# Optimization experiments

Hardware: AMD Instinct MI355X
Metric: run time of the kernel (lower is better)

The kernel has to match this reference:

```python
import jax, jax.numpy as jnp
import numpy as np

B, S, D = 4, 4096, 64   # batch, seq_len, input_size
H, HD = 4, 16           # num_heads, head_dim


def setup_inputs() -> dict:
    key = jax.random.key(0)
    ks = jax.random.split(key, 9)
    sd = 1.0 / np.sqrt(D)          # torch Linear default uniform(-1/sqrt(fan_in), ...)
    so = 1.0 / np.sqrt(H * HD)
    u = lambda k, shape, s: jax.random.uniform(k, shape, jnp.float32, -s, s)
    return {
        "x": jax.random.normal(ks[0], (B, S, D), jnp.float32),
        "Wq": u(ks[1], (H, D, HD), sd), "bq": u(ks[2], (H, HD), sd),
        "Wk": u(ks[3], (H, D, HD), sd), "bk": u(ks[4], (H, HD), sd),
        "Wv": u(ks[5], (H, D, HD), sd), "bv": u(ks[6], (H, HD), sd),
        "Wo": u(ks[7], (H * HD, D), so), "bo": u(ks[8], (D,), so),
    }


def reference(x, Wq, bq, Wk, bk, Wv, bv, Wo, bo):
    # Batched per-head projections (fuses the original per-head Linear loop)
    q = jnp.einsum('bsd,hde->bhse', x, Wq) + bq[None, :, None, :]
    k = jnp.einsum('bsd,hde->bhse', x, Wk) + bk[None, :, None, :]
    v = jnp.einsum('bsd,hde->bhse', x, Wv) + bv[None, :, None, :]
    # scores: [B, H, S(query), S(key)]
    scores = jnp.einsum('bhse,bhte->bhst', q, k) / np.sqrt(HD).astype(np.float32)
    # FAITHFUL quirk: torch Softmax(dim=1) on [B,S,S] normalizes over the QUERY axis
    w = jax.nn.softmax(scores, axis=2)
    attended = jnp.einsum('bhst,bhte->bhse', w, v)          # [B,H,S,HD]
    concat = attended.transpose(0, 2, 1, 3).reshape(B, S, H * HD)
    out = concat @ Wo + bo                                   # [B,S,D]
    # FAITHFUL quirk: final softmax over the sequence axis (dim=1)
    return jax.nn.softmax(out, axis=1)
```

## Files before the change

### kernel.cpp

```cpp
#include <hip/hip_runtime.h>
#include <hip/hip_bf16.h>


#define BB 4
#define SS 4096
#define DD 64
#define HH 4
#define HDD 16

typedef unsigned int u32;
typedef unsigned short u16;
typedef __attribute__((ext_vector_type(8))) short bfrag;
typedef __attribute__((ext_vector_type(4))) float floatx4;
typedef __attribute__((ext_vector_type(16))) float floatx16;
typedef __attribute__((ext_vector_type(2))) u32 u32x2;
typedef __attribute__((ext_vector_type(4))) u32 u32x4;

#define LOG2E 1.4426950408889634074f
#define QSCALE (LOG2E * 0.25f)

__device__ __forceinline__ float fexp2(float x) {
#if __has_builtin(__builtin_amdgcn_exp2f)
  return __builtin_amdgcn_exp2f(x);
#else
  float r; asm("v_exp_f32 %0, %1" : "=v"(r) : "v"(x)); return r;
#endif
}
__device__ __forceinline__ float frcp(float x) {
#if __has_builtin(__builtin_amdgcn_rcpf)
  return __builtin_amdgcn_rcpf(x);
#else
  float r; asm("v_rcp_f32 %0, %1" : "=v"(r) : "v"(x)); return r;
#endif
}

__device__ __forceinline__ u16 f2bf(float f) {
  u32 u = __builtin_bit_cast(u32, f);
  return (u16)((u + 0x7FFFu + ((u >> 16) & 1u)) >> 16);
}
__device__ __forceinline__ u32 pack_bf(float lo, float hi) {
#if __has_builtin(__builtin_amdgcn_perm)
  return __builtin_amdgcn_perm(__builtin_bit_cast(u32, hi),
                               __builtin_bit_cast(u32, lo), 0x07060302u);
#else
  u32 a = __builtin_bit_cast(u32, lo);
  u32 b = __builtin_bit_cast(u32, hi);
  return (a >> 16) | (b & 0xFFFF0000u);
#endif
}

__device__ __forceinline__ void gload_lds16(const u16* g, u16* l) {
  __builtin_amdgcn_global_load_lds(
      (const __attribute__((address_space(1))) void*)(g),
      (__attribute__((address_space(3))) void*)(l), 16, 0, 0);
}

__device__ __forceinline__ int tmap(int c) {
  int c5 = c & 31;
  return (c & ~31) + (c5 & 3) + ((c5 >> 2) & 1) * 8 + ((c5 >> 3) & 1) * 16
       + ((c5 >> 4) & 1) * 4;
}

__global__ __launch_bounds__(256) void k_proj(
    const float* __restrict__ x,
    const float* __restrict__ Wq, const float* __restrict__ bq,
    const float* __restrict__ Wk, const float* __restrict__ bk,
    const float* __restrict__ Wv, const float* __restrict__ bv,
    u16* __restrict__ qb, u16* __restrict__ kb, float* __restrict__ vf)
{
  __shared__ float xs[16 * 64];
  const int tid = threadIdx.x;
  const int blk = blockIdx.x;
  const int b   = blk >> 8;
  const int s0  = (blk & 255) << 4;
  ((float4*)xs)[tid] = ((const float4*)(x + ((size_t)b * SS + s0) * DD))[tid];
  __syncthreads();

  const int col = tid & 63, h = col >> 4, e = col & 15;
  const int rg  = tid >> 6;
  float aq[4] = {0,0,0,0}, ak[4] = {0,0,0,0}, av[4] = {0,0,0,0};
  const int wofs = h * (DD * HDD) + e;
#pragma unroll 4
  for (int d = 0; d < DD; ++d) {
    float wq = Wq[wofs + d * HDD];
    float wk = Wk[wofs + d * HDD];
    float wv = Wv[wofs + d * HDD];
    const float* xr = xs + (rg * 4) * 64 + d;
#pragma unroll
    for (int r = 0; r < 4; ++r) {
      float xv = xr[r * 64];
      aq[r] += xv * wq; ak[r] += xv * wk; av[r] += xv * wv;
    }
  }
  const float bqv = bq[col], bkv = bk[col], bvv = bv[col];
  size_t base = ((size_t)(b * HH + h) * SS + (s0 + rg * 4)) * HDD + e;
#pragma unroll
  for (int r = 0; r < 4; ++r) {
    qb[base + r * HDD] = f2bf((aq[r] + bqv) * QSCALE);
    kb[base + r * HDD] = f2bf(ak[r] + bkv);
    vf[base + r * HDD] = av[r] + bvv;
  }
}

__global__ __launch_bounds__(256, 8) void k_colsum(
    const u16* __restrict__ qb, const u16* __restrict__ kb,
    float* __restrict__ csp)
{
  const int tid = threadIdx.x;
  const int lane = tid & 63, w = tid >> 6;
  const int l31 = lane & 31, hl = lane >> 5;
  const int bh = blockIdx.z, chunk = blockIdx.y;
  const int t0 = blockIdx.x * 128 + w * 32;
  const size_t base = (size_t)bh * (SS * HDD);

  const bfrag kf = *(const bfrag*)(kb + base + (size_t)(t0 + l31) * HDD + hl * 8);
  const u16* qp = qb + base + (size_t)l31 * HDD + hl * 8;
  const floatx16 z16 = {0.f};
  float c0 = 0.f, c1 = 0.f, c2 = 0.f, c3 = 0.f;
  const int s0 = chunk * 1024;
#pragma unroll 2
  for (int s = s0; s < s0 + 1024; s += 32) {
    bfrag qfr = *(const bfrag*)(qp + (size_t)s * HDD);
    floatx16 d = __builtin_amdgcn_mfma_f32_32x32x16_bf16(qfr, kf, z16, 0, 0, 0);
#pragma unroll
    for (int i = 0; i < 4; ++i) {
      c0 += fexp2(d[4 * i + 0]);
      c1 += fexp2(d[4 * i + 1]);
      c2 += fexp2(d[4 * i + 2]);
      c3 += fexp2(d[4 * i + 3]);
    }
  }
  float c = (c0 + c1) + (c2 + c3);
  c += __shfl_xor(c, 32, 64);
  if (hl == 0)
    csp[((size_t)bh * 4 + chunk) * SS + t0 + l31] = c;
}

__global__ __launch_bounds__(256) void k_vprep(
    const float* __restrict__ vf, const float* __restrict__ csp,
    u16* __restrict__ vp)
{
  __shared__ float rcls[256];
  const int tid = threadIdx.x;
  const int chunk = blockIdx.x;
  const int bh = blockIdx.y;
  const int t0 = chunk << 8;
  {
    const float* cp = csp + (size_t)bh * 4 * SS + t0 + tid;
    rcls[tid] = frcp(cp[0] + cp[SS] + cp[2 * SS] + cp[3 * SS]);
  }
  __syncthreads();
  const float* vb = vf + ((size_t)bh * SS + t0) * HDD;
  u16* outb = vp + ((size_t)bh * 16 + chunk) * 4096;
#pragma unroll
  for (int gi = 0; gi < 2; ++gi) {
    const int g = gi * 256 + tid;
    const int e = g >> 5, gg = g & 31;
    const int cbase = (gg ^ (e & 7)) << 3;
    u32 r[4];
#pragma unroll
    for (int jj = 0; jj < 4; ++jj) {
      int ta = tmap(cbase + 2 * jj);
      int tb = tmap(cbase + 2 * jj + 1);
      u16 lo = f2bf(vb[ta * HDD + e] * rcls[ta]);
      u16 hi = f2bf(vb[tb * HDD + e] * rcls[tb]);
      r[jj] = (u32)lo | ((u32)hi << 16);
    }
    u32x4 vv = {r[0], r[1], r[2], r[3]};
    *(u32x4*)(outb + g * 8) = vv;
  }
}

__global__ __launch_bounds__(256, 8) void k_attn(
    const u16* __restrict__ qb, const u16* __restrict__ kb,
    const u16* __restrict__ vp, float* __restrict__ attp)
{
  __shared__ __align__(16) u16 vls[2][4096];
  const int tid  = threadIdx.x;
  const int lane = tid & 63, w = tid >> 6;
  const int l31 = lane & 31, hl = lane >> 5;
  const int bh = blockIdx.z, b = bh >> 2, h = bh & 3;
  const int tq = blockIdx.y;
  const int s0 = blockIdx.x * 128 + w * 32;
  const size_t base = (size_t)bh * (SS * HDD);

  const bfrag qf = *(const bfrag*)(qb + base + (size_t)(s0 + l31) * HDD + hl * 8);
  const u16* kp = kb + base + ((size_t)tq * 1024 + l31) * HDD + hl * 8;
  const floatx16 z16 = {0.f};
  floatx16 acc = {0.f};

  const u16* vsrc = vp + ((size_t)bh * 16 + tq * 4) * 4096;

  {
    const u16* gs = vsrc + w * 1024 + lane * 8;
    u16* ls = &vls[0][0] + w * 1024;
    gload_lds16(gs, ls);
    gload_lds16(gs + 512, ls + 512);
  }
  __syncthreads();

#pragma unroll
  for (int ch = 0; ch < 4; ++ch) {
    if (ch < 3) {
      const u16* gs = vsrc + (ch + 1) * 4096 + w * 1024 + lane * 8;
      u16* ls = &vls[(ch + 1) & 1][0] + w * 1024;
      gload_lds16(gs, ls);
      gload_lds16(gs + 512, ls + 512);
    }

    const u16* vrow = &vls[ch & 1][0] + (l31 & 15) * 256;
    const int eb = l31 & 7;
    const int tb = ch * 256;
#pragma unroll 2
    for (int it = 0; it < 8; ++it) {
      bfrag kf = *(const bfrag*)(kp + (size_t)(tb + it * 32) * HDD);
      floatx16 d = __builtin_amdgcn_mfma_f32_32x32x16_bf16(kf, qf, z16, 0, 0, 0);
      u32 wr[8];
#pragma unroll
      for (int p = 0; p < 8; ++p)
        wr[p] = pack_bf(fexp2(d[2 * p]), fexp2(d[2 * p + 1]));
      const int cc0 = it * 4 + hl * 2;
      u32x4 af0 = *(const u32x4*)(vrow + ((cc0 ^ eb) << 3));
      u32x4 af1 = *(const u32x4*)(vrow + (((cc0 + 1) ^ eb) << 3));
      u32x4 ef0 = {wr[0], wr[1], wr[2], wr[3]};
      u32x4 ef1 = {wr[4], wr[5], wr[6], wr[7]};
      acc = __builtin_amdgcn_mfma_f32_32x32x16_bf16(
          __builtin_bit_cast(bfrag, af0), __builtin_bit_cast(bfrag, ef0), acc, 0, 0, 0);
      acc = __builtin_amdgcn_mfma_f32_32x32x16_bf16(
          __builtin_bit_cast(bfrag, af1), __builtin_bit_cast(bfrag, ef1), acc, 0, 0, 0);
    }
    __syncthreads();
  }

  float* ao = attp + (((size_t)tq * BB + b) * SS + s0 + l31) * (HH * HDD)
            + h * HDD + 4 * hl;
  float4 lo4 = {acc[0], acc[1], acc[2], acc[3]};
  float4 hi4 = {acc[4], acc[5], acc[6], acc[7]};
  *(float4*)ao       = lo4;
  *(float4*)(ao + 8) = hi4;
}

__global__ __launch_bounds__(256) void k_oproj(
    const float* __restrict__ att, const float* __restrict__ Wo,
    const float* __restrict__ bo, float* __restrict__ outp,
    float* __restrict__ part)
{
  __shared__ float wols[64 * 64];
  __shared__ float red[4][64];
  const int tid = threadIdx.x;
  const int blk = blockIdx.x;
  const int b = blk >> 9, s0 = (blk & 511) << 3;
#pragma unroll
  for (int i = 0; i < 4; ++i)
    ((float4*)wols)[tid + 256 * i] = ((const float4*)Wo)[tid + 256 * i];
  __syncthreads();

  const int d = tid & 63, sg = tid >> 6;
  const float bov = bo[d];
  const size_t so = (size_t)BB * SS * 16;
  float es = 0.f;
#pragma unroll
  for (int r = 0; r < 2; ++r) {
    int s = s0 + sg * 2 + r;
    const floatx4* row = (const floatx4*)(att + ((size_t)b * SS + s) * 64);
    float acc = bov;
#pragma unroll
    for (int j = 0; j < 16; ++j) {
      floatx4 c = (row[j] + row[j + so]) + (row[j + 2 * so] + row[j + 3 * so]);
      acc += c[0] * wols[(4*j+0)*64 + d] + c[1] * wols[(4*j+1)*64 + d]
           + c[2] * wols[(4*j+2)*64 + d] + c[3] * wols[(4*j+3)*64 + d];
    }
    outp[((size_t)b * SS + s) * 64 + d] = acc;
    es += fexp2(acc * LOG2E);
  }
  red[sg][d] = es;
  __syncthreads();
  if (tid < 64)
    part[((size_t)b * 512 + (blk & 511)) * 64 + tid] =
        red[0][tid] + red[1][tid] + red[2][tid] + red[3][tid];
}

__global__ __launch_bounds__(256) void k_softmax(
    const float* __restrict__ outp, const float* __restrict__ part,
    float* __restrict__ out)
{
  __shared__ float red[4][64];
  __shared__ float rs[64];
  const int tid = threadIdx.x, d = tid & 63, sg = tid >> 6;
  const int st = blockIdx.x;
  const int b = blockIdx.y;
  {
    float e = 0.f;
    const float* pp = part + ((size_t)b * 512 + sg * 128) * 64 + d;
#pragma unroll 8
    for (int c = 0; c < 128; ++c) e += pp[c * 64];
    red[sg][d] = e;
  }
  __syncthreads();
  if (tid < 64)
    rs[tid] = frcp(red[0][tid] + red[1][tid] + red[2][tid] + red[3][tid]);
  __syncthreads();
  const float r = rs[d];
  const size_t rowbase = ((size_t)b * SS + st * 64 + sg * 16) * 64 + d;
#pragma unroll 4
  for (int i = 0; i < 16; ++i)
    out[rowbase + i * 64] = fexp2(outp[rowbase + i * 64] * LOG2E) * r;
}

extern "C" void kernel_launch(void* const* d_in, const int* in_sizes, int n_in,
                              void* d_out, int out_size, void* d_ws, size_t ws_size,
                              hipStream_t stream) {
  const float* x  = (const float*)d_in[0];
  const float* Wq = (const float*)d_in[1];
  const float* bq = (const float*)d_in[2];
  const float* Wk = (const float*)d_in[3];
  const float* bk = (const float*)d_in[4];
  const float* Wv = (const float*)d_in[5];
  const float* bv = (const float*)d_in[6];
  const float* Wo = (const float*)d_in[7];
  const float* bo = (const float*)d_in[8];

  char* ws = (char*)d_ws;
  constexpr size_t QB_OFF  = 0;
  constexpr size_t KB_OFF  = (size_t)2  << 20;
  constexpr size_t VF_OFF  = (size_t)4  << 20;
  constexpr size_t CSP_OFF = (size_t)8  << 20;
  constexpr size_t VP_OFF  = (size_t)9  << 20;
  constexpr size_t ATT_OFF = (size_t)11 << 20;
  constexpr size_t OUT_OFF = (size_t)27 << 20;
  constexpr size_t PT_OFF  = (size_t)31 << 20;

  u16*   qb   = (u16*)  (ws + QB_OFF);
  u16*   kb   = (u16*)  (ws + KB_OFF);
  float* vf   = (float*)(ws + VF_OFF);
  float* csp  = (float*)(ws + CSP_OFF);
  u16*   vpb  = (u16*)  (ws + VP_OFF);
  float* attp = (float*)(ws + ATT_OFF);
  float* outp = (float*)(ws + OUT_OFF);
  float* part = (float*)(ws + PT_OFF);
  float* out  = (float*)d_out;

  hipLaunchKernelGGL(k_proj,    dim3(1024),       dim3(256), 0, stream,
                     x, Wq, bq, Wk, bk, Wv, bv, qb, kb, vf);
  hipLaunchKernelGGL(k_colsum,  dim3(32, 4, 16),  dim3(256), 0, stream, qb, kb, csp);
  hipLaunchKernelGGL(k_vprep,   dim3(16, 16),     dim3(256), 0, stream, vf, csp, vpb);
  hipLaunchKernelGGL(k_attn,    dim3(32, 4, 16),  dim3(256), 0, stream,
                     qb, kb, vpb, attp);
  hipLaunchKernelGGL(k_oproj,   dim3(2048),       dim3(256), 0, stream,
                     attp, Wo, bo, outp, part);
  hipLaunchKernelGGL(k_softmax, dim3(64, 4),      dim3(256), 0, stream, outp, part, out);
}
```

Before: 206.3 us.

## Halve attention key split, prefetch K fragments, stage V in LDS, pipeline Q loads

```diff
diff --git a/kernel.cpp b/kernel.cpp
--- a/kernel.cpp
+++ b/kernel.cpp
@@ -114,20 +114,25 @@
   const size_t base = (size_t)bh * (SS * HDD);
 
   const bfrag kf = *(const bfrag*)(kb + base + (size_t)(t0 + l31) * HDD + hl * 8);
-  const u16* qp = qb + base + (size_t)l31 * HDD + hl * 8;
+  const u16* qp = qb + base + ((size_t)chunk * 1024 + l31) * HDD + hl * 8;
   const floatx16 z16 = {0.f};
   float c0 = 0.f, c1 = 0.f, c2 = 0.f, c3 = 0.f;
-  const int s0 = chunk * 1024;
-#pragma unroll 2
-  for (int s = s0; s < s0 + 1024; s += 32) {
-    bfrag qfr = *(const bfrag*)(qp + (size_t)s * HDD);
-    floatx16 d = __builtin_amdgcn_mfma_f32_32x32x16_bf16(qfr, kf, z16, 0, 0, 0);
-#pragma unroll
-    for (int i = 0; i < 4; ++i) {
-      c0 += fexp2(d[4 * i + 0]);
-      c1 += fexp2(d[4 * i + 1]);
-      c2 += fexp2(d[4 * i + 2]);
-      c3 += fexp2(d[4 * i + 3]);
+
+  bfrag q2[2];
+  q2[0] = *(const bfrag*)(qp);
+  q2[1] = *(const bfrag*)(qp + (size_t)32 * HDD);
+#pragma unroll 4
+  for (int i = 0; i < 32; ++i) {
+    bfrag qa = q2[i & 1];
+    if (i < 30)
+      q2[i & 1] = *(const bfrag*)(qp + (size_t)((i + 2) * 32) * HDD);
+    floatx16 d = __builtin_amdgcn_mfma_f32_32x32x16_bf16(qa, kf, z16, 0, 0, 0);
+#pragma unroll
+    for (int j = 0; j < 4; ++j) {
+      c0 += fexp2(d[4 * j + 0]);
+      c1 += fexp2(d[4 * j + 1]);
+      c2 += fexp2(d[4 * j + 2]);
+      c3 += fexp2(d[4 * j + 3]);
     }
   }
   float c = (c0 + c1) + (c2 + c3);
@@ -140,17 +145,21 @@
     const float* __restrict__ vf, const float* __restrict__ csp,
     u16* __restrict__ vp)
 {
+  __shared__ float vstage[256 * 16];
   __shared__ float rcls[256];
   const int tid = threadIdx.x;
   const int chunk = blockIdx.x;
   const int bh = blockIdx.y;
   const int t0 = chunk << 8;
   {
+    const float4* src = (const float4*)(vf + ((size_t)bh * SS + t0) * HDD);
+    float4* dst = (float4*)vstage;
+#pragma unroll
+    for (int i = 0; i < 4; ++i) dst[tid + 256 * i] = src[tid + 256 * i];
     const float* cp = csp + (size_t)bh * 4 * SS + t0 + tid;
     rcls[tid] = frcp(cp[0] + cp[SS] + cp[2 * SS] + cp[3 * SS]);
   }
   __syncthreads();
-  const float* vb = vf + ((size_t)bh * SS + t0) * HDD;
   u16* outb = vp + ((size_t)bh * 16 + chunk) * 4096;
 #pragma unroll
   for (int gi = 0; gi < 2; ++gi) {
@@ -162,8 +171,8 @@
     for (int jj = 0; jj < 4; ++jj) {
       int ta = tmap(cbase + 2 * jj);
       int tb = tmap(cbase + 2 * jj + 1);
-      u16 lo = f2bf(vb[ta * HDD + e] * rcls[ta]);
-      u16 hi = f2bf(vb[tb * HDD + e] * rcls[tb]);
+      u16 lo = f2bf(vstage[ta * 16 + e] * rcls[ta]);
+      u16 hi = f2bf(vstage[tb * 16 + e] * rcls[tb]);
       r[jj] = (u32)lo | ((u32)hi << 16);
     }
     u32x4 vv = {r[0], r[1], r[2], r[3]};
@@ -171,7 +180,7 @@
   }
 }
 
-__global__ __launch_bounds__(256, 8) void k_attn(
+__global__ __launch_bounds__(256, 4) void k_attn(
     const u16* __restrict__ qb, const u16* __restrict__ kb,
     const u16* __restrict__ vp, float* __restrict__ attp)
 {
@@ -180,16 +189,16 @@
   const int lane = tid & 63, w = tid >> 6;
   const int l31 = lane & 31, hl = lane >> 5;
   const int bh = blockIdx.z, b = bh >> 2, h = bh & 3;
-  const int tq = blockIdx.y;
+  const int tph = blockIdx.y;
   const int s0 = blockIdx.x * 128 + w * 32;
   const size_t base = (size_t)bh * (SS * HDD);
 
   const bfrag qf = *(const bfrag*)(qb + base + (size_t)(s0 + l31) * HDD + hl * 8);
-  const u16* kp = kb + base + ((size_t)tq * 1024 + l31) * HDD + hl * 8;
+  const u16* kp = kb + base + ((size_t)tph * 2048 + l31) * HDD + hl * 8;
   const floatx16 z16 = {0.f};
   floatx16 acc = {0.f};
 
-  const u16* vsrc = vp + ((size_t)bh * 16 + tq * 4) * 4096;
+  const u16* vsrc = vp + ((size_t)bh * 16 + tph * 8) * 4096;
 
   {
     const u16* gs = vsrc + w * 1024 + lane * 8;
@@ -197,11 +206,15 @@
     gload_lds16(gs, ls);
     gload_lds16(gs + 512, ls + 512);
   }
-  __syncthreads();
-
-#pragma unroll
-  for (int ch = 0; ch < 4; ++ch) {
-    if (ch < 3) {
+  bfrag kfr[8];
+#pragma unroll
+  for (int it = 0; it < 8; ++it)
+    kfr[it] = *(const bfrag*)(kp + (size_t)(it * 32) * HDD);
+  __syncthreads();
+
+#pragma unroll
+  for (int ch = 0; ch < 8; ++ch) {
+    if (ch < 7) {
       const u16* gs = vsrc + (ch + 1) * 4096 + w * 1024 + lane * 8;
       u16* ls = &vls[(ch + 1) & 1][0] + w * 1024;
       gload_lds16(gs, ls);
@@ -210,10 +223,11 @@
 
     const u16* vrow = &vls[ch & 1][0] + (l31 & 15) * 256;
     const int eb = l31 & 7;
-    const int tb = ch * 256;
-#pragma unroll 2
+#pragma unroll
     for (int it = 0; it < 8; ++it) {
-      bfrag kf = *(const bfrag*)(kp + (size_t)(tb + it * 32) * HDD);
+      bfrag kf = kfr[it];
+      if (ch < 7)
+        kfr[it] = *(const bfrag*)(kp + (size_t)((ch + 1) * 256 + it * 32) * HDD);
       floatx16 d = __builtin_amdgcn_mfma_f32_32x32x16_bf16(kf, qf, z16, 0, 0, 0);
       u32 wr[8];
 #pragma unroll
@@ -232,7 +246,7 @@
     __syncthreads();
   }
 
-  float* ao = attp + (((size_t)tq * BB + b) * SS + s0 + l31) * (HH * HDD)
+  float* ao = attp + (((size_t)tph * BB + b) * SS + s0 + l31) * (HH * HDD)
             + h * HDD + 4 * hl;
   float4 lo4 = {acc[0], acc[1], acc[2], acc[3]};
   float4 hi4 = {acc[4], acc[5], acc[6], acc[7]};
@@ -266,7 +280,7 @@
     float acc = bov;
 #pragma unroll
     for (int j = 0; j < 16; ++j) {
-      floatx4 c = (row[j] + row[j + so]) + (row[j + 2 * so] + row[j + 3 * so]);
+      floatx4 c = row[j] + row[j + so];
       acc += c[0] * wols[(4*j+0)*64 + d] + c[1] * wols[(4*j+1)*64 + d]
            + c[2] * wols[(4*j+2)*64 + d] + c[3] * wols[(4*j+3)*64 + d];
     }
@@ -327,8 +341,8 @@
   constexpr size_t CSP_OFF = (size_t)8  << 20;
   constexpr size_t VP_OFF  = (size_t)9  << 20;
   constexpr size_t ATT_OFF = (size_t)11 << 20;
-  constexpr size_t OUT_OFF = (size_t)27 << 20;
-  constexpr size_t PT_OFF  = (size_t)31 << 20;
+  constexpr size_t OUT_OFF = (size_t)19 << 20;
+  constexpr size_t PT_OFF  = (size_t)23 << 20;
 
   u16*   qb   = (u16*)  (ws + QB_OFF);
   u16*   kb   = (u16*)  (ws + KB_OFF);
@@ -344,7 +358,7 @@
                      x, Wq, bq, Wk, bk, Wv, bv, qb, kb, vf);
   hipLaunchKernelGGL(k_colsum,  dim3(32, 4, 16),  dim3(256), 0, stream, qb, kb, csp);
   hipLaunchKernelGGL(k_vprep,   dim3(16, 16),     dim3(256), 0, stream, vf, csp, vpb);
-  hipLaunchKernelGGL(k_attn,    dim3(32, 4, 16),  dim3(256), 0, stream,
+  hipLaunchKernelGGL(k_attn,    dim3(32, 2, 16),  dim3(256), 0, stream,
                      qb, kb, vpb, attp);
   hipLaunchKernelGGL(k_oproj,   dim3(2048),       dim3(256), 0, stream,
                      attp, Wo, bo, outp, part);
```

Result: faster. 202.1 us (-2.0%).
